# Kernel optimization log

Measured on AMD Instinct MI355X. Metric: run time of the kernel, lower is better.

## Reference

```python
import jax, jax.numpy as jnp
import numpy as np

SZ = 256          # image side
K = 4             # neighbors
NUM_CHANNELS = 8
CHUNK = 512       # query chunk for brute-force KNN
BIG = 1e10        # penalty added to squared distance of non-filled candidates


def _fill_channel(img, mask):
    """img: [SZ,SZ] float, mask: [SZ,SZ] bool. Returns filled [SZ,SZ].

    Faithful to TreeMultiRandom: filled pixels = mask nonzero; for every
    unfilled pixel take K nearest filled pixels (Euclidean on coords/SZ,
    i.e. norm_coord) and fill with sum(val_j * dist_j) / sum(dist_j)
    (NOTE: the original weights by distance, not inverse distance; kept as-is).
    Filled pixels keep their (masked) value.
    """
    N = SZ * SZ
    r = jnp.arange(SZ, dtype=jnp.float32) / SZ  # norm_coord
    gy, gx = jnp.meshgrid(r, r, indexing='ij')  # (row, col) like .nonzero()
    py = gy.reshape(N)
    px = gx.reshape(N)
    mflat = mask.reshape(N)
    vflat = (img * mask).reshape(N)  # holed image values
    penalty = jnp.where(mflat, 0.0, BIG).astype(jnp.float32)

    def chunk_fn(q):
        qy, qx = q  # each [CHUNK]
        # masked squared distances to all candidates: [CHUNK, N]
        d2 = (qy[:, None] - py[None, :]) ** 2 + (qx[:, None] - px[None, :]) ** 2 \
             + penalty[None, :]
        neg, idx = jax.lax.top_k(-d2, K)          # K smallest distances
        dist = jnp.sqrt(jnp.maximum(-neg, 0.0))   # [CHUNK, K] (KDTree returns L2)
        v = vflat[idx]                            # gather neighbor values
        return jnp.sum(v * dist, axis=1) / jnp.sum(dist, axis=1)

    qys = py.reshape(-1, CHUNK)
    qxs = px.reshape(-1, CHUNK)
    vals = jax.lax.map(chunk_fn, (qys, qxs)).reshape(N)
    # unfilled pixels get interpolated vals; filled keep holed value
    return jnp.where(mflat, vflat, vals).reshape(SZ, SZ)


def reference(coded, lookup_table):
    img = coded[0, 0]  # [SZ, SZ]
    chans = [_fill_channel(img, lookup_table == c)
             for c in range(1, NUM_CHANNELS + 1)]
    return jnp.stack(chans)[None]  # [1, NUM_CHANNELS, SZ, SZ]


def setup_inputs() -> dict:
    key = jax.random.key(0)
    k1, k2 = jax.random.split(key)
    coded = jax.random.normal(k1, (1, 1, SZ, SZ), dtype=jnp.float32)
    # values in 1..NUM_CHANNELS so every channel has a nonempty filled set
    lookup_table = jax.random.randint(k2, (SZ, SZ), 1, NUM_CHANNELS + 1,
                                      dtype=jnp.int32)
    return {"coded": coded, "lookup_table": lookup_table}
```

## Files before the change

kernel.cpp:

```cpp
#include <hip/hip_runtime.h>
#include <math.h>

#define SZ 256
#define KNN 4
#define NUM_CHANNELS 8
#define R 7
#define WROWS (2 * R + 1)
#define FR 16
#define FROWS (2 * FR + 1)
#define RSTRIDE 6

typedef unsigned long long u64;
typedef unsigned int u32;

__device__ __forceinline__ void ins4(u32 key, u32& k0, u32& k1,
                                     u32& k2, u32& k3) {
    u32 m;
    m = (k2 > key) ? k2 : key;  k3 = (k3 < m) ? k3 : m;
    m = (k1 > key) ? k1 : key;  k2 = (k2 < m) ? k2 : m;
    m = (k0 > key) ? k0 : key;  k1 = (k1 < m) ? k1 : m;
    k0 = (k0 < key) ? k0 : key;
}

__device__ __forceinline__ void ins4_64(u64 key, u64& k0, u64& k1,
                                        u64& k2, u64& k3) {
    if (key < k3) {
        u64 m;
        m = (k2 > key) ? k2 : key;  k3 = (k3 < m) ? k3 : m;
        m = (k1 > key) ? k1 : key;  k2 = (k2 < m) ? k2 : m;
        m = (k0 > key) ? k0 : key;  k1 = (k1 < m) ? k1 : m;
        k0 = (k0 < key) ? k0 : key;
    }
}

__global__ __launch_bounds__(256) void knn_fill(
    const float* __restrict__ img,
    const int*   __restrict__ lut,
    float*       __restrict__ out)
{
    __shared__ u64 win[FROWS * RSTRIDE];

    const int x    = threadIdx.x;
    const int y    = blockIdx.x;
    const int ch   = blockIdx.y;
    const int c    = ch + 1;
    const int lane = x & 63;
    const int w64  = x >> 6;

    int y0b = y - FR;
    if (y0b < 0) y0b = 0;
    if (y0b > SZ - FROWS) y0b = SZ - FROWS;
    int y0m = y - R;
    if (y0m < 0) y0m = 0;
    if (y0m > SZ - WROWS) y0m = SZ - WROWS;
    const int rstart = y0m - y0b;

    if (x < FROWS * 2) win[(x >> 1) * RSTRIDE + (x & 1) * 5] = 0;

    #pragma unroll
    for (int rr = 0; rr < FROWS; ++rr) {
        const int v = lut[(y0b + rr) * SZ + x];
        const u64 bal = __ballot(v == c);
        if (lane == 0) win[rr * RSTRIDE + 1 + w64] = bal;
    }
    __syncthreads();

    const int pix = y * SZ + x;
    float* outc = out + (size_t)ch * (SZ * SZ);

    if ((win[(y - y0b) * RSTRIDE + 1 + (x >> 6)] >> (x & 63)) & 1ull) {
        outc[pix] = img[pix];
        return;
    }

    u32 k0 = ~0u, k1 = ~0u, k2 = ~0u, k3 = ~0u;

    const int base = x - R + 64;
    const int wrd  = base >> 6;
    const int sh   = base & 63;

    #pragma unroll
    for (int rr = 0; rr < WROWS; ++rr) {
        const int rr2 = rstart + rr;
        const u64 lo = win[rr2 * RSTRIDE + wrd];
        const u64 hi = win[rr2 * RSTRIDE + wrd + 1];
        u32 w = (u32)((u64)(((((unsigned __int128)hi) << 64) | lo) >> sh))
                & ((1u << WROWS) - 1);
        const int dy   = y0m + rr - y;
        const int dy2  = dy * dy;
        const int rowx = (y0m + rr) * SZ + x;
        while (w) {
            const int b = __builtin_ctz(w);
            w &= w - 1;
            const int dx  = b - R;
            const u32 d2  = (u32)(dy2 + dx * dx);
            const u32 key = (d2 << 16) | (u32)(rowx + dx);
            ins4(key, k0, k1, k2, k3);
        }
    }

    u64 ks[KNN];
    const u32 in_d2 = k3 >> 16;
    if (in_d2 < (u32)((R + 1) * (R + 1))) {
        ks[0] = k0; ks[1] = k1; ks[2] = k2; ks[3] = k3;
    } else {
        const u32 cap = in_d2;
        u32 q0 = ~0u, q1 = ~0u, q2 = ~0u, q3 = ~0u;
        for (int ady = 0; ady < FROWS; ++ady) {
            u32 cur = q3 >> 16;
            if (cap < cur) cur = cap;
            const u32 a2 = (u32)(ady * ady);
            if (a2 > cur) break;
            const u32 bound = cur - a2;
            int Rx = (bound >= 65025u) ? (SZ - 1)
                                       : ((int)sqrtf((float)bound) + 1);
            int xs = x - Rx; if (xs < 0) xs = 0;
            int xe = x + Rx; if (xe > SZ - 1) xe = SZ - 1;
            const int jxs = xs >> 6, jxe = xe >> 6;
            const u64 mlo = (~0ull) << (xs & 63);
            const u64 mhi = (~0ull) >> (63 - (xe & 63));
            #pragma unroll
            for (int s = 0; s < 2; ++s) {
                if (s && ady == 0) continue;
                const int yy = s ? y + ady : y - ady;
                const int rr2 = yy - y0b;
                if (rr2 < 0 || rr2 >= FROWS) continue;
                const int rb = yy * SZ;
                const u64* rw = &win[rr2 * RSTRIDE + 1];
                for (int j = jxs; j <= jxe; ++j) {
                    u64 w = rw[j];
                    if (j == jxs) w &= mlo;
                    if (j == jxe) w &= mhi;
                    while (w) {
                        const int b = __builtin_ctzll(w);
                        w &= w - 1;
                        const int xx = (j << 6) + b;
                        const int dxx = xx - x;
                        const u32 d2 = a2 + (u32)(dxx * dxx);
                        ins4((d2 << 16) | (u32)(rb + xx), q0, q1, q2, q3);
                    }
                }
            }
        }
        if ((q3 >> 16) < 289u) {
            ks[0] = q0; ks[1] = q1; ks[2] = q2; ks[3] = q3;
        } else {
            const u64 cap2 = (q3 != ~0u) ? (u64)(q3 >> 16) : (~0ull >> 16);
            u64 t0 = ~0ull, t1 = ~0ull, t2 = ~0ull, t3 = ~0ull;
            for (int ady = 0; ady < SZ; ++ady) {
                u64 cur = t3 >> 16;
                if (cap2 < cur) cur = cap2;
                const u64 a2 = (u64)(ady * ady);
                if (a2 > cur) break;
                const u64 bound = cur - a2;
                int Rx = (bound >= 65025ull) ? (SZ - 1)
                                             : ((int)sqrtf((float)bound) + 1);
                int xs = x - Rx; if (xs < 0) xs = 0;
                int xe = x + Rx; if (xe > SZ - 1) xe = SZ - 1;
                for (int s = 0; s < 2; ++s) {
                    if (s && ady == 0) continue;
                    const int yy = s ? y + ady : y - ady;
                    if (yy < 0 || yy > SZ - 1) continue;
                    const int rb = yy * SZ;
                    for (int xx = xs; xx <= xe; ++xx) {
                        if (lut[rb + xx] == c) {
                            const int dxx = xx - x;
                            const u64 d2 = a2 + (u64)(dxx * dxx);
                            ins4_64((d2 << 16) | (u32)(rb + xx),
                                    t0, t1, t2, t3);
                        }
                    }
                }
            }
            ks[0] = t0; ks[1] = t1; ks[2] = t2; ks[3] = t3;
        }
    }

    float num = 0.0f, den = 0.0f;
    #pragma unroll
    for (int i = 0; i < KNN; ++i) {
        const int idx = (int)(ks[i] & 0xFFFFull);
        const int d2i = (int)(ks[i] >> 16);
        const float dist = sqrtf((float)d2i * (1.0f / 65536.0f));
        num += img[idx] * dist;
        den += dist;
    }
    outc[pix] = num / den;
}

extern "C" void kernel_launch(void* const* d_in, const int* in_sizes, int n_in,
                              void* d_out, int out_size, void* d_ws, size_t ws_size,
                              hipStream_t stream) {
    const float* img = (const float*)d_in[0];
    const int*   lut = (const int*)d_in[1];
    float*       out = (float*)d_out;

    knn_fill<<<dim3(SZ, NUM_CHANNELS), dim3(256), 0, stream>>>(img, lut, out);
}
```

Baseline: 79.09 us.

## Precompute per-channel occupancy bitmaps and scan rows outward with early exit

A separate pre-pass builds per-channel 64-bit occupancy bitmaps from the lookup table once. The fill kernel then loads its window from these bitmaps instead of rebuilding it with 33 ballots per block. The local 15-row search now visits rows in order of distance from the query row and stops once the whole wavefront has four neighbours closer than the next ring. The global fallback also scans bitmaps instead of reading the int LUT per pixel. The cost is a second kernel launch plus workspace traffic, and the mid-range search switches to 64-bit keys.

```diff
diff --git a/kernel.cpp b/kernel.cpp
--- a/kernel.cpp
+++ b/kernel.cpp
@@ -33,19 +33,34 @@
     }
 }
 
+__global__ __launch_bounds__(256) void build_bitmaps(
+    const int* __restrict__ lut,
+    u64* __restrict__ bm)
+{
+    const int y = blockIdx.x;
+    const int x = threadIdx.x;
+    const int v = lut[y * SZ + x];
+    const int lane = x & 63;
+    const int w64 = x >> 6;
+    #pragma unroll
+    for (int c = 1; c <= NUM_CHANNELS; ++c) {
+        u64 bal = __ballot(v == c);
+        if (lane == 0) bm[(size_t)(c - 1) * (SZ * 4) + y * 4 + w64] = bal;
+    }
+}
+
 __global__ __launch_bounds__(256) void knn_fill(
     const float* __restrict__ img,
-    const int*   __restrict__ lut,
+    const u64*   __restrict__ bm,
     float*       __restrict__ out)
 {
     __shared__ u64 win[FROWS * RSTRIDE];
 
-    const int x    = threadIdx.x;
-    const int y    = blockIdx.x;
-    const int ch   = blockIdx.y;
-    const int c    = ch + 1;
-    const int lane = x & 63;
-    const int w64  = x >> 6;
+    const int x   = threadIdx.x;
+    const int y   = blockIdx.x;
+    const int ch  = blockIdx.y;
+    const int tid = threadIdx.x;
+    const u64* bmc = bm + (size_t)ch * (SZ * 4);
 
     int y0b = y - FR;
     if (y0b < 0) y0b = 0;
@@ -53,15 +68,12 @@
     int y0m = y - R;
     if (y0m < 0) y0m = 0;
     if (y0m > SZ - WROWS) y0m = SZ - WROWS;
-    const int rstart = y0m - y0b;
-
-    if (x < FROWS * 2) win[(x >> 1) * RSTRIDE + (x & 1) * 5] = 0;
-
-    #pragma unroll
-    for (int rr = 0; rr < FROWS; ++rr) {
-        const int v = lut[(y0b + rr) * SZ + x];
-        const u64 bal = __ballot(v == c);
-        if (lane == 0) win[rr * RSTRIDE + 1 + w64] = bal;
+    const int m0 = y0m - y0b;
+
+    if (tid < FROWS * 2) win[(tid >> 1) * RSTRIDE + (tid & 1) * 5] = 0;
+    if (tid < FROWS * 4) {
+        const int rr = tid >> 2, j = tid & 3;
+        win[rr * RSTRIDE + 1 + j] = bmc[(y0b + rr) * 4 + j];
     }
     __syncthreads();
 
@@ -79,24 +91,30 @@
     const int wrd  = base >> 6;
     const int sh   = base & 63;
 
-    #pragma unroll
-    for (int rr = 0; rr < WROWS; ++rr) {
-        const int rr2 = rstart + rr;
-        const u64 lo = win[rr2 * RSTRIDE + wrd];
-        const u64 hi = win[rr2 * RSTRIDE + wrd + 1];
-        u32 w = (u32)((u64)(((((unsigned __int128)hi) << 64) | lo) >> sh))
-                & ((1u << WROWS) - 1);
-        const int dy   = y0m + rr - y;
-        const int dy2  = dy * dy;
-        const int rowx = (y0m + rr) * SZ + x;
-        while (w) {
-            const int b = __builtin_ctz(w);
-            w &= w - 1;
-            const int dx  = b - R;
-            const u32 d2  = (u32)(dy2 + dx * dx);
-            const u32 key = (d2 << 16) | (u32)(rowx + dx);
-            ins4(key, k0, k1, k2, k3);
+    for (int ady = 0; ady < WROWS; ++ady) {
+        #pragma unroll
+        for (int s = 0; s < 2; ++s) {
+            if (s && ady == 0) continue;
+            const int yy = s ? y + ady : y - ady;
+            const int rr = yy - y0m;
+            if (rr < 0 || rr >= WROWS) continue;
+            const int rr2 = m0 + rr;
+            const u64 lo = win[rr2 * RSTRIDE + wrd];
+            const u64 hi = win[rr2 * RSTRIDE + wrd + 1];
+            u32 w = (u32)((u64)(((((unsigned __int128)hi) << 64) | lo) >> sh))
+                    & ((1u << WROWS) - 1);
+            const int dy2  = ady * ady;
+            const int rowx = yy * SZ + x;
+            while (w) {
+                const int b = __builtin_ctz(w);
+                w &= w - 1;
+                const int dx  = b - R;
+                const u32 d2  = (u32)(dy2 + dx * dx);
+                const u32 key = (d2 << 16) | (u32)(rowx + dx);
+                ins4(key, k0, k1, k2, k3);
+            }
         }
+        if (__all((k3 >> 16) < (u32)((ady + 1) * (ady + 1)))) break;
     }
 
     u64 ks[KNN];
@@ -104,16 +122,16 @@
     if (in_d2 < (u32)((R + 1) * (R + 1))) {
         ks[0] = k0; ks[1] = k1; ks[2] = k2; ks[3] = k3;
     } else {
-        const u32 cap = in_d2;
-        u32 q0 = ~0u, q1 = ~0u, q2 = ~0u, q3 = ~0u;
+        const u64 cap = (u64)in_d2;
+        u64 q0 = ~0ull, q1 = ~0ull, q2 = ~0ull, q3 = ~0ull;
         for (int ady = 0; ady < FROWS; ++ady) {
-            u32 cur = q3 >> 16;
+            u64 cur = q3 >> 16;
             if (cap < cur) cur = cap;
-            const u32 a2 = (u32)(ady * ady);
+            const u64 a2 = (u64)(ady * ady);
             if (a2 > cur) break;
-            const u32 bound = cur - a2;
-            int Rx = (bound >= 65025u) ? (SZ - 1)
-                                       : ((int)sqrtf((float)bound) + 1);
+            const u64 bound = cur - a2;
+            int Rx = (bound >= 65025ull) ? (SZ - 1)
+                                         : ((int)sqrtf((float)bound) + 1);
             int xs = x - Rx; if (xs < 0) xs = 0;
             int xe = x + Rx; if (xe > SZ - 1) xe = SZ - 1;
             const int jxs = xs >> 6, jxe = xe >> 6;
@@ -136,16 +154,16 @@
                         w &= w - 1;
                         const int xx = (j << 6) + b;
                         const int dxx = xx - x;
-                        const u32 d2 = a2 + (u32)(dxx * dxx);
-                        ins4((d2 << 16) | (u32)(rb + xx), q0, q1, q2, q3);
+                        const u64 d2 = a2 + (u64)(dxx * dxx);
+                        ins4_64((d2 << 16) | (u32)(rb + xx), q0, q1, q2, q3);
                     }
                 }
             }
         }
-        if ((q3 >> 16) < 289u) {
+        if ((q3 >> 16) < 289ull) {
             ks[0] = q0; ks[1] = q1; ks[2] = q2; ks[3] = q3;
         } else {
-            const u64 cap2 = (q3 != ~0u) ? (u64)(q3 >> 16) : (~0ull >> 16);
+            const u64 cap2 = q3 >> 16;
             u64 t0 = ~0ull, t1 = ~0ull, t2 = ~0ull, t3 = ~0ull;
             for (int ady = 0; ady < SZ; ++ady) {
                 u64 cur = t3 >> 16;
@@ -157,13 +175,22 @@
                                              : ((int)sqrtf((float)bound) + 1);
                 int xs = x - Rx; if (xs < 0) xs = 0;
                 int xe = x + Rx; if (xe > SZ - 1) xe = SZ - 1;
+                const int jxs = xs >> 6, jxe = xe >> 6;
+                const u64 mlo = (~0ull) << (xs & 63);
+                const u64 mhi = (~0ull) >> (63 - (xe & 63));
                 for (int s = 0; s < 2; ++s) {
                     if (s && ady == 0) continue;
                     const int yy = s ? y + ady : y - ady;
                     if (yy < 0 || yy > SZ - 1) continue;
                     const int rb = yy * SZ;
-                    for (int xx = xs; xx <= xe; ++xx) {
-                        if (lut[rb + xx] == c) {
+                    for (int j = jxs; j <= jxe; ++j) {
+                        u64 w = bmc[yy * 4 + j];
+                        if (j == jxs) w &= mlo;
+                        if (j == jxe) w &= mhi;
+                        while (w) {
+                            const int b = __builtin_ctzll(w);
+                            w &= w - 1;
+                            const int xx = (j << 6) + b;
                             const int dxx = xx - x;
                             const u64 d2 = a2 + (u64)(dxx * dxx);
                             ins4_64((d2 << 16) | (u32)(rb + xx),
@@ -194,6 +221,8 @@
     const float* img = (const float*)d_in[0];
     const int*   lut = (const int*)d_in[1];
     float*       out = (float*)d_out;
-
-    knn_fill<<<dim3(SZ, NUM_CHANNELS), dim3(256), 0, stream>>>(img, lut, out);
-}
+    u64*         bm  = (u64*)d_ws;
+
+    build_bitmaps<<<dim3(SZ), dim3(256), 0, stream>>>(lut, bm);
+    knn_fill<<<dim3(SZ, NUM_CHANNELS), dim3(256), 0, stream>>>(img, bm, out);
+}
```

New measurement: 72.17 us (median of 2 runs). 1.1x faster.

## Load fallback window lazily and early-exit inner KNN scan by row distance

Applied to the files above, without the earlier changes.

Only the 15 rows of the inner window are balloted into shared memory up front. The remaining rows of the 33-row window are loaded only when some pixel in the block needs the wider search, which is signalled through a shared flag. The inner search now walks rows outward from the query row and stops once every lane in the wave has its fourth neighbour closer than the next row distance. Filled pixels stay in the loop until the barriers, and the mid-tier search is widened to 64-bit keys. This adds an extra __syncthreads and a block-wide flag, and the __all early exit adds a wave vote per row.

```diff
diff --git a/kernel.cpp b/kernel.cpp
--- a/kernel.cpp
+++ b/kernel.cpp
@@ -39,6 +39,7 @@
     float*       __restrict__ out)
 {
     __shared__ u64 win[FROWS * RSTRIDE];
+    __shared__ int fbflag;
 
     const int x    = threadIdx.x;
     const int y    = blockIdx.x;
@@ -53,25 +54,24 @@
     int y0m = y - R;
     if (y0m < 0) y0m = 0;
     if (y0m > SZ - WROWS) y0m = SZ - WROWS;
-    const int rstart = y0m - y0b;
+    const int m0 = y0m - y0b;
 
     if (x < FROWS * 2) win[(x >> 1) * RSTRIDE + (x & 1) * 5] = 0;
+    if (x == 0) fbflag = 0;
 
     #pragma unroll
-    for (int rr = 0; rr < FROWS; ++rr) {
-        const int v = lut[(y0b + rr) * SZ + x];
+    for (int rr = 0; rr < WROWS; ++rr) {
+        const int v = lut[(y0m + rr) * SZ + x];
         const u64 bal = __ballot(v == c);
-        if (lane == 0) win[rr * RSTRIDE + 1 + w64] = bal;
+        if (lane == 0) win[(m0 + rr) * RSTRIDE + 1 + w64] = bal;
     }
     __syncthreads();
 
     const int pix = y * SZ + x;
     float* outc = out + (size_t)ch * (SZ * SZ);
 
-    if ((win[(y - y0b) * RSTRIDE + 1 + (x >> 6)] >> (x & 63)) & 1ull) {
-        outc[pix] = img[pix];
-        return;
-    }
+    const bool filled =
+        (win[(y - y0b) * RSTRIDE + 1 + (x >> 6)] >> (x & 63)) & 1ull;
 
     u32 k0 = ~0u, k1 = ~0u, k2 = ~0u, k3 = ~0u;
 
@@ -79,41 +79,69 @@
     const int wrd  = base >> 6;
     const int sh   = base & 63;
 
-    #pragma unroll
-    for (int rr = 0; rr < WROWS; ++rr) {
-        const int rr2 = rstart + rr;
-        const u64 lo = win[rr2 * RSTRIDE + wrd];
-        const u64 hi = win[rr2 * RSTRIDE + wrd + 1];
-        u32 w = (u32)((u64)(((((unsigned __int128)hi) << 64) | lo) >> sh))
-                & ((1u << WROWS) - 1);
-        const int dy   = y0m + rr - y;
-        const int dy2  = dy * dy;
-        const int rowx = (y0m + rr) * SZ + x;
-        while (w) {
-            const int b = __builtin_ctz(w);
-            w &= w - 1;
-            const int dx  = b - R;
-            const u32 d2  = (u32)(dy2 + dx * dx);
-            const u32 key = (d2 << 16) | (u32)(rowx + dx);
-            ins4(key, k0, k1, k2, k3);
-        }
+    if (!filled) {
+        for (int ady = 0; ady < WROWS; ++ady) {
+            #pragma unroll
+            for (int s = 0; s < 2; ++s) {
+                if (s && ady == 0) continue;
+                const int yy = s ? y + ady : y - ady;
+                const int rr = yy - y0m;
+                if (rr < 0 || rr >= WROWS) continue;
+                const int rr2 = m0 + rr;
+                const u64 lo = win[rr2 * RSTRIDE + wrd];
+                const u64 hi = win[rr2 * RSTRIDE + wrd + 1];
+                u32 w = (u32)((u64)(((((unsigned __int128)hi) << 64) | lo)
+                                    >> sh)) & ((1u << WROWS) - 1);
+                const int dy2  = ady * ady;
+                const int rowx = yy * SZ + x;
+                while (w) {
+                    const int b = __builtin_ctz(w);
+                    w &= w - 1;
+                    const int dx  = b - R;
+                    const u32 d2  = (u32)(dy2 + dx * dx);
+                    const u32 key = (d2 << 16) | (u32)(rowx + dx);
+                    ins4(key, k0, k1, k2, k3);
+                }
+            }
+            if (__all((k3 >> 16) < (u32)((ady + 1) * (ady + 1)))) break;
+        }
+    }
+
+    const u32 in_d2 = k3 >> 16;
+    const bool need = !filled && in_d2 >= (u32)((R + 1) * (R + 1));
+    if (need) fbflag = 1;
+    __syncthreads();
+
+    if (fbflag) {
+        #pragma unroll
+        for (int rr = 0; rr < FROWS; ++rr) {
+            if (rr >= m0 && rr < m0 + WROWS) continue;
+            const int v = lut[(y0b + rr) * SZ + x];
+            const u64 bal = __ballot(v == c);
+            if (lane == 0) win[rr * RSTRIDE + 1 + w64] = bal;
+        }
+        __syncthreads();
+    }
+
+    if (filled) {
+        outc[pix] = img[pix];
+        return;
     }
 
     u64 ks[KNN];
-    const u32 in_d2 = k3 >> 16;
-    if (in_d2 < (u32)((R + 1) * (R + 1))) {
+    if (!need) {
         ks[0] = k0; ks[1] = k1; ks[2] = k2; ks[3] = k3;
     } else {
-        const u32 cap = in_d2;
-        u32 q0 = ~0u, q1 = ~0u, q2 = ~0u, q3 = ~0u;
+        const u64 cap = (u64)in_d2;
+        u64 q0 = ~0ull, q1 = ~0ull, q2 = ~0ull, q3 = ~0ull;
         for (int ady = 0; ady < FROWS; ++ady) {
-            u32 cur = q3 >> 16;
+            u64 cur = q3 >> 16;
             if (cap < cur) cur = cap;
-            const u32 a2 = (u32)(ady * ady);
+            const u64 a2 = (u64)(ady * ady);
             if (a2 > cur) break;
-            const u32 bound = cur - a2;
-            int Rx = (bound >= 65025u) ? (SZ - 1)
-                                       : ((int)sqrtf((float)bound) + 1);
+            const u64 bound = cur - a2;
+            int Rx = (bound >= 65025ull) ? (SZ - 1)
+                                         : ((int)sqrtf((float)bound) + 1);
             int xs = x - Rx; if (xs < 0) xs = 0;
             int xe = x + Rx; if (xe > SZ - 1) xe = SZ - 1;
             const int jxs = xs >> 6, jxe = xe >> 6;
@@ -136,16 +164,16 @@
                         w &= w - 1;
                         const int xx = (j << 6) + b;
                         const int dxx = xx - x;
-                        const u32 d2 = a2 + (u32)(dxx * dxx);
-                        ins4((d2 << 16) | (u32)(rb + xx), q0, q1, q2, q3);
+                        const u64 d2 = a2 + (u64)(dxx * dxx);
+                        ins4_64((d2 << 16) | (u32)(rb + xx), q0, q1, q2, q3);
                     }
                 }
             }
         }
-        if ((q3 >> 16) < 289u) {
+        if ((q3 >> 16) < 289ull) {
             ks[0] = q0; ks[1] = q1; ks[2] = q2; ks[3] = q3;
         } else {
-            const u64 cap2 = (q3 != ~0u) ? (u64)(q3 >> 16) : (~0ull >> 16);
+            const u64 cap2 = q3 >> 16;
             u64 t0 = ~0ull, t1 = ~0ull, t2 = ~0ull, t3 = ~0ull;
             for (int ady = 0; ady < SZ; ++ady) {
                 u64 cur = t3 >> 16;
```

After: 75.38 us. -4.7%, faster.
